# Kernel tuning notes

Measured on AMD Instinct MI355X. Metric: run time of the kernel, lower is better.

The kernel has to match this reference:

```python
import jax, jax.numpy as jnp
import numpy as np

L, R = -0.1, 1.1          # HardKuma stretched support
MAX_REL = 11              # max relative distance
CLAMP_LO, CLAMP_HI = 0.01, 100.0


def setup_inputs() -> dict:
    key = jax.random.key(0)
    ks = jax.random.split(key, 12)
    B, T, Din, Dout = 4, 2048, 512, 256
    s_in = 0.02
    return {
        "q": jax.random.normal(ks[0], (B, T, Din), jnp.float32),
        "k": jax.random.normal(ks[1], (B, T, Din), jnp.float32),
        "Wa1": jax.random.normal(ks[2], (Din, Dout), jnp.float32) * s_in,
        "ba1": jnp.zeros((Dout,), jnp.float32),
        "Wa2": jax.random.normal(ks[3], (Dout, Dout), jnp.float32) * s_in,
        "ba2": jnp.zeros((Dout,), jnp.float32),
        "Wb1": jax.random.normal(ks[4], (Din, Dout), jnp.float32) * s_in,
        "bb1": jnp.zeros((Dout,), jnp.float32),
        "Wb2": jax.random.normal(ks[5], (Dout, Dout), jnp.float32) * s_in,
        "bb2": jnp.zeros((Dout,), jnp.float32),
        "dist_emb": jax.random.normal(ks[6], (2 * MAX_REL + 1,), jnp.float32) * 0.02,
    }


def _mlp(x, W1, b1, W2, b2):
    # Sequential(Linear, ReLU, Dropout, Linear, ReLU, Dropout) in eval mode
    h = jax.nn.relu(x @ W1 + b1)
    return jax.nn.relu(h @ W2 + b2)


def _rel_dists(T, dist_emb):
    i = jnp.arange(T)
    rel = jnp.clip(i[None, :] - i[:, None], -MAX_REL, MAX_REL) + MAX_REL  # [T,T] ints in [0,22]
    return dist_emb[rel]  # [T,T]


def _kuma_cdf(t, a, b):
    # F(t; a, b) = 1 - (1 - t^a)^b, t is a positive Python-float constant
    return 1.0 - jnp.power(1.0 - jnp.power(t, a), b)


def _kuma_mean(a, b):
    # E[X] = b * Beta(1 + 1/a, b)
    g = 1.0 + 1.0 / a
    return b * jnp.exp(jax.scipy.special.gammaln(g) + jax.scipy.special.gammaln(b)
                       - jax.scipy.special.gammaln(g + b))


def reference(q, k, Wa1, ba1, Wa2, ba2, Wb1, bb1, Wb2, bb2, dist_emb):
    T = q.shape[1]
    q_a = _mlp(q, Wa1, ba1, Wa2, ba2)
    k_a = _mlp(k, Wa1, ba1, Wa2, ba2)
    q_b = _mlp(q, Wb1, bb1, Wb2, bb2)
    k_b = _mlp(k, Wb1, bb1, Wb2, bb2)

    a = jnp.einsum("btd,bsd->bts", q_a, k_a)  # [B,T,T]
    b = jnp.einsum("btd,bsd->bts", q_b, k_b)

    rd = _rel_dists(T, dist_emb)[None]  # [1,T,T]
    a = a + rd
    b = b + rd

    a = jnp.clip(jax.nn.softplus(a), CLAMP_LO, CLAMP_HI)
    b = jnp.clip(jax.nn.softplus(b), CLAMP_LO, CLAMP_HI)

    # HardKuma deterministic (eval) attention
    t0 = (0.0 - L) / (R - L)  # stretched coord of 0
    t1 = (1.0 - L) / (R - L)  # stretched coord of 1
    p0 = _kuma_cdf(t0, a, b)          # P(h = 0)
    p1 = 1.0 - _kuma_cdf(t1, a, b)    # P(h = 1)
    pc = 1.0 - p0 - p1                # continuous mass

    mean = jnp.clip(L + (R - L) * _kuma_mean(a, b), 0.0, 1.0)
    zero_one = jnp.where(p0 > p1, 0.0, 1.0)
    att = jnp.where(pc < 0.5, zero_one, mean)
    return att
```

## Files before the change

### kernel.cpp

```cpp
#include <hip/hip_runtime.h>
#include <hip/hip_bf16.h>
#include <math.h>

typedef __hip_bfloat16 bf16;
typedef short bf16x8 __attribute__((ext_vector_type(8)));
typedef float f32x4 __attribute__((ext_vector_type(4)));
typedef float f32x2 __attribute__((ext_vector_type(2)));

union alignas(16) Pack8 { bf16 h[8]; bf16x8 v; };

#define EXP2F(x) __builtin_amdgcn_exp2f(x)
#define LOG2F(x) __builtin_amdgcn_logf(x)
#define RCPF(x)  __builtin_amdgcn_rcpf(x)

#define TAB_N   64
#define TAB_LO  (-0.35f)
#define TAB_HI  (1.25f)
#define TAB_STRIDE 65

__global__ void prep_weights(const float* __restrict__ Wa1, const float* __restrict__ Wa2,
                             const float* __restrict__ Wb1, const float* __restrict__ Wb2,
                             bf16* __restrict__ oa1, bf16* __restrict__ oa2,
                             bf16* __restrict__ ob1, bf16* __restrict__ ob2) {
    int idx = blockIdx.x * 256 + threadIdx.x;
    if (idx < 131072) {
        int n = idx >> 9, k = idx & 511;
        oa1[idx] = __float2bfloat16(Wa1[k * 256 + n]);
    } else if (idx < 196608) {
        int i = idx - 131072; int n = i >> 8, k = i & 255;
        oa2[i] = __float2bfloat16(Wa2[k * 256 + n]);
    } else if (idx < 327680) {
        int i = idx - 196608; int n = i >> 9, k = i & 511;
        ob1[i] = __float2bfloat16(Wb1[k * 256 + n]);
    } else {
        int i = idx - 327680; int n = i >> 8, k = i & 255;
        ob2[i] = __float2bfloat16(Wb2[k * 256 + n]);
    }
}

__device__ __forceinline__ float stirl2s(float z) {
    float iz = 1.f / z;
    return (z - 0.5f) * LOG2F(z) - 1.44269504f * z + 1.32574806f
         + iz * (0.12022651f - 0.00400749f * iz * iz);
}
__device__ __forceinline__ float sp4s(float x) {
    return (x * (x + 1.f)) * ((x + 2.f) * (x + 3.f));
}
__device__ float mean_f32(float sa, float sb) {
    float lw = LOG2F(1.f + EXP2F(sa * 1.44269504f));
    float lv = LOG2F(1.f + EXP2F(sb * 1.44269504f));
    lw = fminf(fmaxf(lw, 0.01442695f), 144.269504f);
    lv = fminf(fmaxf(lv, 0.01442695f), 144.269504f);
    float b = 0.69314718f * lv;
    float g = 1.44269504f / lw + 1.f;
    float gb = g + b;
    float lb2 = stirl2s(g + 4.f) + stirl2s(b + 4.f) - stirl2s(gb + 4.f)
              + LOG2F(sp4s(gb) / (sp4s(g) * sp4s(b)));
    float mean = fmaf(1.2f * b, EXP2F(lb2), -0.1f);
    return fminf(fmaxf(mean, 0.f), 1.f);
}

__global__ void gen_table(float* __restrict__ tab) {
    int idx = blockIdx.x * 256 + threadIdx.x;
    if (idx >= TAB_N * TAB_N) return;
    int ia = idx >> 6, ib = idx & 63;
    const float step = (TAB_HI - TAB_LO) / (TAB_N - 1);
    float sa  = TAB_LO + ia * step;
    float sb  = TAB_LO + ib * step;
    int ib1 = ib < TAB_N - 1 ? ib + 1 : ib;
    float sb1 = TAB_LO + ib1 * step;
    tab[(ia * TAB_STRIDE + ib) * 2]     = mean_f32(sa, sb);
    tab[(ia * TAB_STRIDE + ib) * 2 + 1] = mean_f32(sa, sb1);
}

__global__ __launch_bounds__(256, 2)
void mlp_fused(const float* __restrict__ q, const float* __restrict__ k,
               const bf16* __restrict__ Wa1t, const bf16* __restrict__ Wa2t,
               const bf16* __restrict__ Wb1t, const bf16* __restrict__ Wb2t,
               bf16* __restrict__ qa, bf16* __restrict__ ka,
               bf16* __restrict__ qb, bf16* __restrict__ kb) {
    const int z = blockIdx.z;
    const float* X  = (z & 1) ? k : q;
    const bf16*  W1 = (z >> 1) ? Wb1t : Wa1t;
    const bf16*  W2 = (z >> 1) ? Wb2t : Wa2t;
    bf16* Y = (z == 0) ? qa : (z == 1) ? ka : (z == 2) ? qb : kb;
    const int m0 = blockIdx.x * 64;

    __shared__ short lA[64 * 40];
    __shared__ short lB[256 * 40];
    __shared__ short lH[64 * 264];

    const int tid  = threadIdx.x;
    const int wave = tid >> 6, lane = tid & 63;
    const int wn = wave * 64;
    const int quad = lane >> 4, r16 = lane & 15;

    {
        f32x4 acc[4][4] = {};
        for (int kk = 0; kk < 512; kk += 32) {
            {
                int r = tid >> 2, c = (tid & 3) * 8;
                const float* p = X + (size_t)(m0 + r) * 512 + kk + c;
                Pack8 u;
#pragma unroll
                for (int j = 0; j < 8; j++) u.h[j] = __float2bfloat16(p[j]);
                *(bf16x8*)&lA[r * 40 + c] = u.v;
            }
            for (int i = tid; i < 1024; i += 256) {
                int r = i >> 2, c = (i & 3) * 8;
                *(bf16x8*)&lB[r * 40 + c] =
                    *(const bf16x8*)(W1 + (size_t)r * 512 + kk + c);
            }
            __syncthreads();
            bf16x8 af[4], bfr[4];
#pragma unroll
            for (int f = 0; f < 4; f++) {
                af[f]  = *(const bf16x8*)&lA[(f * 16 + r16) * 40 + quad * 8];
                bfr[f] = *(const bf16x8*)&lB[(wn + f * 16 + r16) * 40 + quad * 8];
            }
#pragma unroll
            for (int i = 0; i < 4; i++)
#pragma unroll
                for (int j = 0; j < 4; j++)
                    acc[i][j] = __builtin_amdgcn_mfma_f32_16x16x32_bf16(
                        af[i], bfr[j], acc[i][j], 0, 0, 0);
            __syncthreads();
        }
#pragma unroll
        for (int i = 0; i < 4; i++)
#pragma unroll
            for (int j = 0; j < 4; j++)
#pragma unroll
                for (int r = 0; r < 4; r++) {
                    float v = acc[i][j][r];
                    v = v > 0.f ? v : 0.f;
                    ((bf16*)lH)[(i * 16 + quad * 4 + r) * 264 + wn + j * 16 + r16] =
                        __float2bfloat16(v);
                }
    }
    __syncthreads();

    f32x4 acc2[4][4] = {};
    for (int kk = 0; kk < 256; kk += 32) {
        for (int i = tid; i < 1024; i += 256) {
            int r = i >> 2, c = (i & 3) * 8;
            *(bf16x8*)&lB[r * 40 + c] =
                *(const bf16x8*)(W2 + (size_t)r * 256 + kk + c);
        }
        __syncthreads();
        bf16x8 af[4], bfr[4];
#pragma unroll
        for (int f = 0; f < 4; f++) {
            af[f]  = *(const bf16x8*)&lH[(f * 16 + r16) * 264 + kk + quad * 8];
            bfr[f] = *(const bf16x8*)&lB[(wn + f * 16 + r16) * 40 + quad * 8];
        }
#pragma unroll
        for (int i = 0; i < 4; i++)
#pragma unroll
            for (int j = 0; j < 4; j++)
                acc2[i][j] = __builtin_amdgcn_mfma_f32_16x16x32_bf16(
                    af[i], bfr[j], acc2[i][j], 0, 0, 0);
        __syncthreads();
    }

#pragma unroll
    for (int i = 0; i < 4; i++) {
        int rbase = m0 + i * 16 + quad * 4;
#pragma unroll
        for (int j = 0; j < 4; j++) {
            int col = wn + j * 16 + r16;
#pragma unroll
            for (int r = 0; r < 4; r++) {
                float v = acc2[i][j][r];
                v = v > 0.f ? v : 0.f;
                Y[(size_t)(rbase + r) * 256 + col] = __float2bfloat16(v);
            }
        }
    }
}

__device__ __forceinline__ f32x2 vexp2(f32x2 x) {
    f32x2 r; r.x = EXP2F(x.x); r.y = EXP2F(x.y); return r;
}
__device__ __forceinline__ f32x2 vlog2(f32x2 x) {
    f32x2 r; r.x = LOG2F(x.x); r.y = LOG2F(x.y); return r;
}
__device__ __forceinline__ f32x2 vrcp(f32x2 x) {
    f32x2 r; r.x = RCPF(x.x); r.y = RCPF(x.y); return r;
}
__device__ __forceinline__ f32x2 vclamp(f32x2 x, float lo, float hi) {
    f32x2 r;
    r.x = fminf(fmaxf(x.x, lo), hi);
    r.y = fminf(fmaxf(x.y, lo), hi);
    return r;
}

__device__ __noinline__ f32x2 hardkuma_slow(f32x2 la, f32x2 lb) {
    const float LOG2E = 1.44269504f;
    f32x2 lw = vlog2(1.f + vexp2(la * LOG2E));
    f32x2 lv = vlog2(1.f + vexp2(lb * LOG2E));
    lw = vclamp(lw, 0.01442695f, 144.269504f);
    lv = vclamp(lv, 0.01442695f, 144.269504f);
    f32x2 b = 0.69314718f * lv;

    f32x2 t0a = vexp2(-2.48490665f * lw);
    f32x2 t1a = vexp2(-0.08701138f * lw);
    f32x2 q0 = vexp2(b * vlog2(1.f - t0a));
    f32x2 p1 = vexp2(b * vlog2(1.f - t1a));
    f32x2 pc = q0 - p1;
    f32x2 p0 = 1.f - q0;

    f32x2 g  = 1.44269504f * vrcp(lw) + 1.f;
    f32x2 gb = g + b;
    f32x2 g2 = g + 2.f, b2 = b + 2.f, gb2 = gb + 2.f;

    f32x2 s = (g + 1.5f) * vlog2(g2) + (b + 1.5f) * vlog2(b2)
            - (gb + 1.5f) * vlog2(gb2);

    const float C1 = 0.12022459f;
    const float C2 = -0.00400749f;
    f32x2 pg  = g2 * b2;
    f32x2 rr3 = vrcp(pg * gb2);
    f32x2 ig  = rr3 * (b2 * gb2);
    f32x2 ib  = rr3 * (g2 * gb2);
    f32x2 igb = rr3 * pg;
    f32x2 corr = ig  * (C1 + C2 * (ig  * ig))
               + ib  * (C1 + C2 * (ib  * ib))
               - igb * (C1 + C2 * (igb * igb));
    s += corr - 1.55964202f;

    f32x2 ng = g * (g + 1.f), nb = b * (b + 1.f), ngb = gb * (gb + 1.f);
    s += vlog2(ngb * vrcp(ng * nb));

    f32x2 mean = (1.2f * b) * vexp2(s) - 0.1f;
    mean = vclamp(mean, 0.f, 1.f);

    f32x2 att;
    att.x = (pc.x < 0.5f) ? ((p0.x > p1.x) ? 0.f : 1.f) : mean.x;
    att.y = (pc.y < 0.5f) ? ((p0.y > p1.y) ? 0.f : 1.f) : mean.y;
    return att;
}

__global__ __launch_bounds__(256, 2)
void kuma_attn(const bf16* __restrict__ qa, const bf16* __restrict__ ka,
               const bf16* __restrict__ qb, const bf16* __restrict__ kb,
               const float* __restrict__ dist_emb, const float* __restrict__ tabg,
               float* __restrict__ out) {
    const int bidx = blockIdx.z;
    const int t0 = blockIdx.x * 128;
    const int s0 = blockIdx.y * 128;

    __shared__ short lQa[128 * 40], lQb[128 * 40];
    __shared__ short lKa[128 * 40], lKb[128 * 40];
    __shared__ float sDist[23];
    __shared__ float sTab[TAB_N * TAB_STRIDE * 2];

    const int tid = threadIdx.x;
    if (tid < 23) sDist[tid] = dist_emb[tid];
    for (int i = tid; i < (TAB_N * TAB_STRIDE * 2) / 4; i += 256)
        ((f32x4*)sTab)[i] = ((const f32x4*)tabg)[i];

    const int wave = tid >> 6, lane = tid & 63;
    const int wm = (wave >> 1) * 64, wn = (wave & 1) * 64;
    const int quad = lane >> 4, r16 = lane & 15;
    const size_t base = (size_t)bidx * 2048 * 256;

    f32x4 accA[4][4] = {};
    f32x4 accB[4][4] = {};

    const int r0 = tid >> 2, c0 = (tid & 3) * 8;
    const int r1 = r0 + 64,  c1 = c0;

    for (int kk = 0; kk < 256; kk += 32) {
        {
            size_t gq0 = base + (size_t)(t0 + r0) * 256 + kk + c0;
            size_t gq1 = base + (size_t)(t0 + r1) * 256 + kk + c1;
            *(bf16x8*)&lQa[r0 * 40 + c0] = *(const bf16x8*)(qa + gq0);
            *(bf16x8*)&lQb[r0 * 40 + c0] = *(const bf16x8*)(qb + gq0);
            *(bf16x8*)&lQa[r1 * 40 + c1] = *(const bf16x8*)(qa + gq1);
            *(bf16x8*)&lQb[r1 * 40 + c1] = *(const bf16x8*)(qb + gq1);
            size_t gk0 = base + (size_t)(s0 + r0) * 256 + kk + c0;
            size_t gk1 = base + (size_t)(s0 + r1) * 256 + kk + c1;
            *(bf16x8*)&lKa[r0 * 40 + c0] = *(const bf16x8*)(ka + gk0);
            *(bf16x8*)&lKb[r0 * 40 + c0] = *(const bf16x8*)(kb + gk0);
            *(bf16x8*)&lKa[r1 * 40 + c1] = *(const bf16x8*)(ka + gk1);
            *(bf16x8*)&lKb[r1 * 40 + c1] = *(const bf16x8*)(kb + gk1);
        }
        __syncthreads();
        bf16x8 aA[4], aB[4], bA[4], bB[4];
#pragma unroll
        for (int f = 0; f < 4; f++) {
            int ar = (wm + f * 16 + r16) * 40 + quad * 8;
            aA[f] = *(const bf16x8*)&lQa[ar];
            aB[f] = *(const bf16x8*)&lQb[ar];
            int br = (wn + f * 16 + r16) * 40 + quad * 8;
            bA[f] = *(const bf16x8*)&lKa[br];
            bB[f] = *(const bf16x8*)&lKb[br];
        }
#pragma unroll
        for (int i = 0; i < 4; i++)
#pragma unroll
            for (int j = 0; j < 4; j++) {
                accA[i][j] = __builtin_amdgcn_mfma_f32_16x16x32_bf16(
                    aA[i], bA[j], accA[i][j], 0, 0, 0);
                accB[i][j] = __builtin_amdgcn_mfma_f32_16x16x32_bf16(
                    aB[i], bB[j], accB[i][j], 0, 0, 0);
            }
        __syncthreads();
    }

    const float SCALE = (TAB_N - 1) / (TAB_HI - TAB_LO);
#pragma unroll
    for (int i = 0; i < 4; i++) {
#pragma unroll
        for (int j = 0; j < 4; j++) {
            int s = s0 + wn + j * 16 + r16;
#pragma unroll
            for (int rr = 0; rr < 2; rr++) {
                int t = t0 + wm + i * 16 + quad * 4 + rr * 2;
                int d0 = s - t;
                int d1 = d0 - 1;
                d0 = d0 < -11 ? -11 : (d0 > 11 ? 11 : d0);
                d1 = d1 < -11 ? -11 : (d1 > 11 ? 11 : d1);
                float rd0 = sDist[d0 + 11];
                float rd1 = sDist[d1 + 11];
                f32x2 la  = { accA[i][j][rr * 2] + rd0, accA[i][j][rr * 2 + 1] + rd1 };
                f32x2 lbv = { accB[i][j][rr * 2] + rd0, accB[i][j][rr * 2 + 1] + rd1 };

                float mn = fminf(fminf(la.x, la.y), fminf(lbv.x, lbv.y));
                float mx = fmaxf(fmaxf(la.x, la.y), fmaxf(lbv.x, lbv.y));

                f32x2 u = vclamp((la  - TAB_LO) * SCALE, 0.f, (float)(TAB_N - 1));
                f32x2 v = vclamp((lbv - TAB_LO) * SCALE, 0.f, (float)(TAB_N - 1));
                int ia0 = (int)u.x; ia0 = ia0 > TAB_N - 2 ? TAB_N - 2 : ia0;
                int ia1 = (int)u.y; ia1 = ia1 > TAB_N - 2 ? TAB_N - 2 : ia1;
                int ib0 = (int)v.x; ib0 = ib0 > TAB_N - 2 ? TAB_N - 2 : ib0;
                int ib1 = (int)v.y; ib1 = ib1 > TAB_N - 2 ? TAB_N - 2 : ib1;
                f32x2 fa = { u.x - (float)ia0, u.y - (float)ia1 };
                f32x2 fb = { v.x - (float)ib0, v.y - (float)ib1 };
                int o0 = (ia0 * TAB_STRIDE + ib0) * 2;
                int o1 = (ia1 * TAB_STRIDE + ib1) * 2;
                f32x2 e0r0 = *(const f32x2*)&sTab[o0];
                f32x2 e0r1 = *(const f32x2*)&sTab[o0 + TAB_STRIDE * 2];
                f32x2 e1r0 = *(const f32x2*)&sTab[o1];
                f32x2 e1r1 = *(const f32x2*)&sTab[o1 + TAB_STRIDE * 2];
                f32x2 m0 = { e0r0.x + fb.x * (e0r0.y - e0r0.x),
                             e1r0.x + fb.y * (e1r0.y - e1r0.x) };
                f32x2 m1 = { e0r1.x + fb.x * (e0r1.y - e0r1.x),
                             e1r1.x + fb.y * (e1r1.y - e1r1.x) };
                f32x2 att = m0 + fa * (m1 - m0);

                bool oob = (mn < TAB_LO) | (mx > TAB_HI);
                if (__builtin_expect(__any(oob), 0)) {
                    f32x2 ex = hardkuma_slow(la, lbv);
                    if (oob) att = ex;
                }

                out[((size_t)bidx * 2048 + t) * 2048 + s] = att.x;
                out[((size_t)bidx * 2048 + t + 1) * 2048 + s] = att.y;
            }
        }
    }
}

extern "C" void kernel_launch(void* const* d_in, const int* in_sizes, int n_in,
                              void* d_out, int out_size, void* d_ws, size_t ws_size,
                              hipStream_t stream) {
    const float* q    = (const float*)d_in[0];
    const float* k    = (const float*)d_in[1];
    const float* Wa1  = (const float*)d_in[2];
    const float* Wa2  = (const float*)d_in[4];
    const float* Wb1  = (const float*)d_in[6];
    const float* Wb2  = (const float*)d_in[8];
    const float* dist = (const float*)d_in[10];
    float* out = (float*)d_out;

    bf16* wsbf = (bf16*)d_ws;
    bf16* Wa1t = wsbf;
    bf16* Wa2t = Wa1t + 131072;
    bf16* Wb1t = Wa2t + 65536;
    bf16* Wb2t = Wb1t + 131072;
    bf16* qa   = Wb2t + 65536;
    bf16* ka   = qa + 2097152;
    bf16* qb   = ka + 2097152;
    bf16* kb   = qb + 2097152;
    float* tabg = (float*)Wa1t;

    prep_weights<<<1536, 256, 0, stream>>>(Wa1, Wa2, Wb1, Wb2,
                                           Wa1t, Wa2t, Wb1t, Wb2t);

    dim3 g1(128, 1, 4), blk(256, 1, 1);
    mlp_fused<<<g1, blk, 0, stream>>>(q, k, Wa1t, Wa2t, Wb1t, Wb2t,
                                      qa, ka, qb, kb);

    gen_table<<<16, 256, 0, stream>>>(tabg);

    dim3 g2(16, 16, 4);
    kuma_attn<<<g2, blk, 0, stream>>>(qa, ka, qb, kb, dist, tabg, out);
}
```

Measured before the change: 197.0 us.

## Merge table generation into weight prep, load MLP operands directly, prefetch attention tiles

```diff
diff --git a/kernel.cpp b/kernel.cpp
--- a/kernel.cpp
+++ b/kernel.cpp
@@ -18,10 +18,46 @@
 #define TAB_HI  (1.25f)
 #define TAB_STRIDE 65
 
+__device__ __forceinline__ float stirl2s(float z) {
+    float iz = 1.f / z;
+    return (z - 0.5f) * LOG2F(z) - 1.44269504f * z + 1.32574806f
+         + iz * (0.12022651f - 0.00400749f * iz * iz);
+}
+__device__ __forceinline__ float sp4s(float x) {
+    return (x * (x + 1.f)) * ((x + 2.f) * (x + 3.f));
+}
+__device__ float mean_f32(float sa, float sb) {
+    float lw = LOG2F(1.f + EXP2F(sa * 1.44269504f));
+    float lv = LOG2F(1.f + EXP2F(sb * 1.44269504f));
+    lw = fminf(fmaxf(lw, 0.01442695f), 144.269504f);
+    lv = fminf(fmaxf(lv, 0.01442695f), 144.269504f);
+    float b = 0.69314718f * lv;
+    float g = 1.44269504f / lw + 1.f;
+    float gb = g + b;
+    float lb2 = stirl2s(g + 4.f) + stirl2s(b + 4.f) - stirl2s(gb + 4.f)
+              + LOG2F(sp4s(gb) / (sp4s(g) * sp4s(b)));
+    float mean = fmaf(1.2f * b, EXP2F(lb2), -0.1f);
+    return fminf(fmaxf(mean, 0.f), 1.f);
+}
+
 __global__ void prep_weights(const float* __restrict__ Wa1, const float* __restrict__ Wa2,
                              const float* __restrict__ Wb1, const float* __restrict__ Wb2,
                              bf16* __restrict__ oa1, bf16* __restrict__ oa2,
-                             bf16* __restrict__ ob1, bf16* __restrict__ ob2) {
+                             bf16* __restrict__ ob1, bf16* __restrict__ ob2,
+                             float* __restrict__ tab) {
+    if (blockIdx.x >= 1536) {
+        int idx = (blockIdx.x - 1536) * 256 + threadIdx.x;
+        if (idx >= TAB_N * TAB_N) return;
+        int ia = idx >> 6, ib = idx & 63;
+        const float step = (TAB_HI - TAB_LO) / (TAB_N - 1);
+        float sa  = TAB_LO + ia * step;
+        float sb  = TAB_LO + ib * step;
+        int ib1 = ib < TAB_N - 1 ? ib + 1 : ib;
+        float sb1 = TAB_LO + ib1 * step;
+        tab[(ia * TAB_STRIDE + ib) * 2]     = mean_f32(sa, sb);
+        tab[(ia * TAB_STRIDE + ib) * 2 + 1] = mean_f32(sa, sb1);
+        return;
+    }
     int idx = blockIdx.x * 256 + threadIdx.x;
     if (idx < 131072) {
         int n = idx >> 9, k = idx & 511;
@@ -38,42 +74,7 @@
     }
 }
 
-__device__ __forceinline__ float stirl2s(float z) {
-    float iz = 1.f / z;
-    return (z - 0.5f) * LOG2F(z) - 1.44269504f * z + 1.32574806f
-         + iz * (0.12022651f - 0.00400749f * iz * iz);
-}
-__device__ __forceinline__ float sp4s(float x) {
-    return (x * (x + 1.f)) * ((x + 2.f) * (x + 3.f));
-}
-__device__ float mean_f32(float sa, float sb) {
-    float lw = LOG2F(1.f + EXP2F(sa * 1.44269504f));
-    float lv = LOG2F(1.f + EXP2F(sb * 1.44269504f));
-    lw = fminf(fmaxf(lw, 0.01442695f), 144.269504f);
-    lv = fminf(fmaxf(lv, 0.01442695f), 144.269504f);
-    float b = 0.69314718f * lv;
-    float g = 1.44269504f / lw + 1.f;
-    float gb = g + b;
-    float lb2 = stirl2s(g + 4.f) + stirl2s(b + 4.f) - stirl2s(gb + 4.f)
-              + LOG2F(sp4s(gb) / (sp4s(g) * sp4s(b)));
-    float mean = fmaf(1.2f * b, EXP2F(lb2), -0.1f);
-    return fminf(fmaxf(mean, 0.f), 1.f);
-}
-
-__global__ void gen_table(float* __restrict__ tab) {
-    int idx = blockIdx.x * 256 + threadIdx.x;
-    if (idx >= TAB_N * TAB_N) return;
-    int ia = idx >> 6, ib = idx & 63;
-    const float step = (TAB_HI - TAB_LO) / (TAB_N - 1);
-    float sa  = TAB_LO + ia * step;
-    float sb  = TAB_LO + ib * step;
-    int ib1 = ib < TAB_N - 1 ? ib + 1 : ib;
-    float sb1 = TAB_LO + ib1 * step;
-    tab[(ia * TAB_STRIDE + ib) * 2]     = mean_f32(sa, sb);
-    tab[(ia * TAB_STRIDE + ib) * 2 + 1] = mean_f32(sa, sb1);
-}
-
-__global__ __launch_bounds__(256, 2)
+__global__ __launch_bounds__(256, 3)
 void mlp_fused(const float* __restrict__ q, const float* __restrict__ k,
                const bf16* __restrict__ Wa1t, const bf16* __restrict__ Wa2t,
                const bf16* __restrict__ Wb1t, const bf16* __restrict__ Wb2t,
@@ -86,8 +87,6 @@
     bf16* Y = (z == 0) ? qa : (z == 1) ? ka : (z == 2) ? qb : kb;
     const int m0 = blockIdx.x * 64;
 
-    __shared__ short lA[64 * 40];
-    __shared__ short lB[256 * 40];
     __shared__ short lH[64 * 264];
 
     const int tid  = threadIdx.x;
@@ -97,26 +96,19 @@
 
     {
         f32x4 acc[4][4] = {};
+        const float* xb = X + (size_t)(m0 + r16) * 512 + quad * 8;
+        const bf16*  wb = W1 + (size_t)(wn + r16) * 512 + quad * 8;
+#pragma unroll 4
         for (int kk = 0; kk < 512; kk += 32) {
-            {
-                int r = tid >> 2, c = (tid & 3) * 8;
-                const float* p = X + (size_t)(m0 + r) * 512 + kk + c;
+            bf16x8 af[4], bfr[4];
+#pragma unroll
+            for (int f = 0; f < 4; f++) {
+                const float* p = xb + (size_t)f * 16 * 512 + kk;
                 Pack8 u;
 #pragma unroll
                 for (int j = 0; j < 8; j++) u.h[j] = __float2bfloat16(p[j]);
-                *(bf16x8*)&lA[r * 40 + c] = u.v;
-            }
-            for (int i = tid; i < 1024; i += 256) {
-                int r = i >> 2, c = (i & 3) * 8;
-                *(bf16x8*)&lB[r * 40 + c] =
-                    *(const bf16x8*)(W1 + (size_t)r * 512 + kk + c);
-            }
-            __syncthreads();
-            bf16x8 af[4], bfr[4];
-#pragma unroll
-            for (int f = 0; f < 4; f++) {
-                af[f]  = *(const bf16x8*)&lA[(f * 16 + r16) * 40 + quad * 8];
-                bfr[f] = *(const bf16x8*)&lB[(wn + f * 16 + r16) * 40 + quad * 8];
+                af[f] = u.v;
+                bfr[f] = *(const bf16x8*)(wb + (size_t)f * 16 * 512 + kk);
             }
 #pragma unroll
             for (int i = 0; i < 4; i++)
@@ -124,7 +116,6 @@
                 for (int j = 0; j < 4; j++)
                     acc[i][j] = __builtin_amdgcn_mfma_f32_16x16x32_bf16(
                         af[i], bfr[j], acc[i][j], 0, 0, 0);
-            __syncthreads();
         }
 #pragma unroll
         for (int i = 0; i < 4; i++)
@@ -141,26 +132,23 @@
     __syncthreads();
 
     f32x4 acc2[4][4] = {};
-    for (int kk = 0; kk < 256; kk += 32) {
-        for (int i = tid; i < 1024; i += 256) {
-            int r = i >> 2, c = (i & 3) * 8;
-            *(bf16x8*)&lB[r * 40 + c] =
-                *(const bf16x8*)(W2 + (size_t)r * 256 + kk + c);
+    {
+        const bf16* wb = W2 + (size_t)(wn + r16) * 256 + quad * 8;
+#pragma unroll 2
+        for (int kk = 0; kk < 256; kk += 32) {
+            bf16x8 af[4], bfr[4];
+#pragma unroll
+            for (int f = 0; f < 4; f++) {
+                af[f]  = *(const bf16x8*)&lH[(f * 16 + r16) * 264 + kk + quad * 8];
+                bfr[f] = *(const bf16x8*)(wb + (size_t)f * 16 * 256 + kk);
+            }
+#pragma unroll
+            for (int i = 0; i < 4; i++)
+#pragma unroll
+                for (int j = 0; j < 4; j++)
+                    acc2[i][j] = __builtin_amdgcn_mfma_f32_16x16x32_bf16(
+                        af[i], bfr[j], acc2[i][j], 0, 0, 0);
         }
-        __syncthreads();
-        bf16x8 af[4], bfr[4];
-#pragma unroll
-        for (int f = 0; f < 4; f++) {
-            af[f]  = *(const bf16x8*)&lH[(f * 16 + r16) * 264 + kk + quad * 8];
-            bfr[f] = *(const bf16x8*)&lB[(wn + f * 16 + r16) * 40 + quad * 8];
-        }
-#pragma unroll
-        for (int i = 0; i < 4; i++)
-#pragma unroll
-            for (int j = 0; j < 4; j++)
-                acc2[i][j] = __builtin_amdgcn_mfma_f32_16x16x32_bf16(
-                    af[i], bfr[j], acc2[i][j], 0, 0, 0);
-        __syncthreads();
     }
 
 #pragma unroll
@@ -269,24 +257,37 @@
     f32x4 accB[4][4] = {};
 
     const int r0 = tid >> 2, c0 = (tid & 3) * 8;
-    const int r1 = r0 + 64,  c1 = c0;
-
+    const int r1 = r0 + 64;
+
+    bf16x8 rQa0, rQa1, rQb0, rQb1, rKa0, rKa1, rKb0, rKb1;
+    auto prefetch = [&](int kk) {
+        size_t gq0 = base + (size_t)(t0 + r0) * 256 + kk + c0;
+        size_t gq1 = base + (size_t)(t0 + r1) * 256 + kk + c0;
+        size_t gk0 = base + (size_t)(s0 + r0) * 256 + kk + c0;
+        size_t gk1 = base + (size_t)(s0 + r1) * 256 + kk + c0;
+        rQa0 = *(const bf16x8*)(qa + gq0);
+        rQa1 = *(const bf16x8*)(qa + gq1);
+        rQb0 = *(const bf16x8*)(qb + gq0);
+        rQb1 = *(const bf16x8*)(qb + gq1);
+        rKa0 = *(const bf16x8*)(ka + gk0);
+        rKa1 = *(const bf16x8*)(ka + gk1);
+        rKb0 = *(const bf16x8*)(kb + gk0);
+        rKb1 = *(const bf16x8*)(kb + gk1);
+    };
+    prefetch(0);
+
+#pragma unroll
     for (int kk = 0; kk < 256; kk += 32) {
-        {
-            size_t gq0 = base + (size_t)(t0 + r0) * 256 + kk + c0;
-            size_t gq1 = base + (size_t)(t0 + r1) * 256 + kk + c1;
-            *(bf16x8*)&lQa[r0 * 40 + c0] = *(const bf16x8*)(qa + gq0);
-            *(bf16x8*)&lQb[r0 * 40 + c0] = *(const bf16x8*)(qb + gq0);
-            *(bf16x8*)&lQa[r1 * 40 + c1] = *(const bf16x8*)(qa + gq1);
-            *(bf16x8*)&lQb[r1 * 40 + c1] = *(const bf16x8*)(qb + gq1);
-            size_t gk0 = base + (size_t)(s0 + r0) * 256 + kk + c0;
-            size_t gk1 = base + (size_t)(s0 + r1) * 256 + kk + c1;
-            *(bf16x8*)&lKa[r0 * 40 + c0] = *(const bf16x8*)(ka + gk0);
-            *(bf16x8*)&lKb[r0 * 40 + c0] = *(const bf16x8*)(kb + gk0);
-            *(bf16x8*)&lKa[r1 * 40 + c1] = *(const bf16x8*)(ka + gk1);
-            *(bf16x8*)&lKb[r1 * 40 + c1] = *(const bf16x8*)(kb + gk1);
-        }
+        *(bf16x8*)&lQa[r0 * 40 + c0] = rQa0;
+        *(bf16x8*)&lQa[r1 * 40 + c0] = rQa1;
+        *(bf16x8*)&lQb[r0 * 40 + c0] = rQb0;
+        *(bf16x8*)&lQb[r1 * 40 + c0] = rQb1;
+        *(bf16x8*)&lKa[r0 * 40 + c0] = rKa0;
+        *(bf16x8*)&lKa[r1 * 40 + c0] = rKa1;
+        *(bf16x8*)&lKb[r0 * 40 + c0] = rKb0;
+        *(bf16x8*)&lKb[r1 * 40 + c0] = rKb1;
         __syncthreads();
+        if (kk < 224) prefetch(kk + 32);
         bf16x8 aA[4], aB[4], bA[4], bB[4];
 #pragma unroll
         for (int f = 0; f < 4; f++) {
@@ -384,17 +385,16 @@
     bf16* ka   = qa + 2097152;
     bf16* qb   = ka + 2097152;
     bf16* kb   = qb + 2097152;
-    float* tabg = (float*)Wa1t;
-
-    prep_weights<<<1536, 256, 0, stream>>>(Wa1, Wa2, Wb1, Wb2,
-                                           Wa1t, Wa2t, Wb1t, Wb2t);
+    bf16* tabr = kb + 2097152;
+    float* tabg = (float*)tabr;
+
+    prep_weights<<<1552, 256, 0, stream>>>(Wa1, Wa2, Wb1, Wb2,
+                                           Wa1t, Wa2t, Wb1t, Wb2t, tabg);
 
     dim3 g1(128, 1, 4), blk(256, 1, 1);
     mlp_fused<<<g1, blk, 0, stream>>>(q, k, Wa1t, Wa2t, Wb1t, Wb2t,
                                       qa, ka, qb, kb);
 
-    gen_table<<<16, 256, 0, stream>>>(tabg);
-
     dim3 g2(16, 16, 4);
     kuma_attn<<<g2, blk, 0, stream>>>(qa, ka, qb, kb, dist, tabg, out);
 }
```

Result: slower. 211.9 us (+7.6%).

## Fuse all stages into one persistent kernel with atomic grid barriers

Applied to the files above, without the earlier changes.

```diff
diff --git a/kernel.cpp b/kernel.cpp
--- a/kernel.cpp
+++ b/kernel.cpp
@@ -18,25 +18,8 @@
 #define TAB_HI  (1.25f)
 #define TAB_STRIDE 65
 
-__global__ void prep_weights(const float* __restrict__ Wa1, const float* __restrict__ Wa2,
-                             const float* __restrict__ Wb1, const float* __restrict__ Wb2,
-                             bf16* __restrict__ oa1, bf16* __restrict__ oa2,
-                             bf16* __restrict__ ob1, bf16* __restrict__ ob2) {
-    int idx = blockIdx.x * 256 + threadIdx.x;
-    if (idx < 131072) {
-        int n = idx >> 9, k = idx & 511;
-        oa1[idx] = __float2bfloat16(Wa1[k * 256 + n]);
-    } else if (idx < 196608) {
-        int i = idx - 131072; int n = i >> 8, k = i & 255;
-        oa2[i] = __float2bfloat16(Wa2[k * 256 + n]);
-    } else if (idx < 327680) {
-        int i = idx - 196608; int n = i >> 9, k = i & 511;
-        ob1[i] = __float2bfloat16(Wb1[k * 256 + n]);
-    } else {
-        int i = idx - 327680; int n = i >> 8, k = i & 255;
-        ob2[i] = __float2bfloat16(Wb2[k * 256 + n]);
-    }
-}
+#define NBLK 512
+
 
 __device__ __forceinline__ float stirl2s(float z) {
     float iz = 1.f / z;
@@ -60,125 +43,6 @@
     return fminf(fmaxf(mean, 0.f), 1.f);
 }
 
-__global__ void gen_table(float* __restrict__ tab) {
-    int idx = blockIdx.x * 256 + threadIdx.x;
-    if (idx >= TAB_N * TAB_N) return;
-    int ia = idx >> 6, ib = idx & 63;
-    const float step = (TAB_HI - TAB_LO) / (TAB_N - 1);
-    float sa  = TAB_LO + ia * step;
-    float sb  = TAB_LO + ib * step;
-    int ib1 = ib < TAB_N - 1 ? ib + 1 : ib;
-    float sb1 = TAB_LO + ib1 * step;
-    tab[(ia * TAB_STRIDE + ib) * 2]     = mean_f32(sa, sb);
-    tab[(ia * TAB_STRIDE + ib) * 2 + 1] = mean_f32(sa, sb1);
-}
-
-__global__ __launch_bounds__(256, 2)
-void mlp_fused(const float* __restrict__ q, const float* __restrict__ k,
-               const bf16* __restrict__ Wa1t, const bf16* __restrict__ Wa2t,
-               const bf16* __restrict__ Wb1t, const bf16* __restrict__ Wb2t,
-               bf16* __restrict__ qa, bf16* __restrict__ ka,
-               bf16* __restrict__ qb, bf16* __restrict__ kb) {
-    const int z = blockIdx.z;
-    const float* X  = (z & 1) ? k : q;
-    const bf16*  W1 = (z >> 1) ? Wb1t : Wa1t;
-    const bf16*  W2 = (z >> 1) ? Wb2t : Wa2t;
-    bf16* Y = (z == 0) ? qa : (z == 1) ? ka : (z == 2) ? qb : kb;
-    const int m0 = blockIdx.x * 64;
-
-    __shared__ short lA[64 * 40];
-    __shared__ short lB[256 * 40];
-    __shared__ short lH[64 * 264];
-
-    const int tid  = threadIdx.x;
-    const int wave = tid >> 6, lane = tid & 63;
-    const int wn = wave * 64;
-    const int quad = lane >> 4, r16 = lane & 15;
-
-    {
-        f32x4 acc[4][4] = {};
-        for (int kk = 0; kk < 512; kk += 32) {
-            {
-                int r = tid >> 2, c = (tid & 3) * 8;
-                const float* p = X + (size_t)(m0 + r) * 512 + kk + c;
-                Pack8 u;
-#pragma unroll
-                for (int j = 0; j < 8; j++) u.h[j] = __float2bfloat16(p[j]);
-                *(bf16x8*)&lA[r * 40 + c] = u.v;
-            }
-            for (int i = tid; i < 1024; i += 256) {
-                int r = i >> 2, c = (i & 3) * 8;
-                *(bf16x8*)&lB[r * 40 + c] =
-                    *(const bf16x8*)(W1 + (size_t)r * 512 + kk + c);
-            }
-            __syncthreads();
-            bf16x8 af[4], bfr[4];
-#pragma unroll
-            for (int f = 0; f < 4; f++) {
-                af[f]  = *(const bf16x8*)&lA[(f * 16 + r16) * 40 + quad * 8];
-                bfr[f] = *(const bf16x8*)&lB[(wn + f * 16 + r16) * 40 + quad * 8];
-            }
-#pragma unroll
-            for (int i = 0; i < 4; i++)
-#pragma unroll
-                for (int j = 0; j < 4; j++)
-                    acc[i][j] = __builtin_amdgcn_mfma_f32_16x16x32_bf16(
-                        af[i], bfr[j], acc[i][j], 0, 0, 0);
-            __syncthreads();
-        }
-#pragma unroll
-        for (int i = 0; i < 4; i++)
-#pragma unroll
-            for (int j = 0; j < 4; j++)
-#pragma unroll
-                for (int r = 0; r < 4; r++) {
-                    float v = acc[i][j][r];
-                    v = v > 0.f ? v : 0.f;
-                    ((bf16*)lH)[(i * 16 + quad * 4 + r) * 264 + wn + j * 16 + r16] =
-                        __float2bfloat16(v);
-                }
-    }
-    __syncthreads();
-
-    f32x4 acc2[4][4] = {};
-    for (int kk = 0; kk < 256; kk += 32) {
-        for (int i = tid; i < 1024; i += 256) {
-            int r = i >> 2, c = (i & 3) * 8;
-            *(bf16x8*)&lB[r * 40 + c] =
-                *(const bf16x8*)(W2 + (size_t)r * 256 + kk + c);
-        }
-        __syncthreads();
-        bf16x8 af[4], bfr[4];
-#pragma unroll
-        for (int f = 0; f < 4; f++) {
-            af[f]  = *(const bf16x8*)&lH[(f * 16 + r16) * 264 + kk + quad * 8];
-            bfr[f] = *(const bf16x8*)&lB[(wn + f * 16 + r16) * 40 + quad * 8];
-        }
-#pragma unroll
-        for (int i = 0; i < 4; i++)
-#pragma unroll
-            for (int j = 0; j < 4; j++)
-                acc2[i][j] = __builtin_amdgcn_mfma_f32_16x16x32_bf16(
-                    af[i], bfr[j], acc2[i][j], 0, 0, 0);
-        __syncthreads();
-    }
-
-#pragma unroll
-    for (int i = 0; i < 4; i++) {
-        int rbase = m0 + i * 16 + quad * 4;
-#pragma unroll
-        for (int j = 0; j < 4; j++) {
-            int col = wn + j * 16 + r16;
-#pragma unroll
-            for (int r = 0; r < 4; r++) {
-                float v = acc2[i][j][r];
-                v = v > 0.f ? v : 0.f;
-                Y[(size_t)(rbase + r) * 256 + col] = __float2bfloat16(v);
-            }
-        }
-    }
-}
-
 __device__ __forceinline__ f32x2 vexp2(f32x2 x) {
     f32x2 r; r.x = EXP2F(x.x); r.y = EXP2F(x.y); return r;
 }
@@ -241,123 +105,297 @@
     return att;
 }
 
+__device__ __forceinline__ void grid_sync(unsigned* cnt) {
+    __syncthreads();
+    if (threadIdx.x == 0) {
+        __threadfence();
+        atomicAdd(cnt, 1u);
+        while (atomicAdd(cnt, 0u) < NBLK) __builtin_amdgcn_s_sleep(8);
+        __threadfence();
+    }
+    __syncthreads();
+}
+
+__device__ __forceinline__ void transpose_tile(const float* __restrict__ src,
+                                               bf16* __restrict__ dst,
+                                               int K, int N, int kt, int nt,
+                                               float* tile ) {
+    const int tid = threadIdx.x;
+    const int tx = tid & 31, ty = tid >> 5;
+    const int k0 = kt * 32, n0 = nt * 32;
+#pragma unroll
+    for (int i = 0; i < 4; i++)
+        tile[(ty + 8 * i) * 33 + tx] = src[(size_t)(k0 + ty + 8 * i) * N + n0 + tx];
+    __syncthreads();
+#pragma unroll
+    for (int i = 0; i < 4; i++)
+        dst[(size_t)(n0 + ty + 8 * i) * K + k0 + tx] =
+            __float2bfloat16(tile[tx * 33 + ty + 8 * i]);
+}
+
 __global__ __launch_bounds__(256, 2)
-void kuma_attn(const bf16* __restrict__ qa, const bf16* __restrict__ ka,
-               const bf16* __restrict__ qb, const bf16* __restrict__ kb,
-               const float* __restrict__ dist_emb, const float* __restrict__ tabg,
+void fused_all(const float* __restrict__ q, const float* __restrict__ k,
+               const float* __restrict__ Wa1, const float* __restrict__ Wa2,
+               const float* __restrict__ Wb1, const float* __restrict__ Wb2,
+               const float* __restrict__ dist_emb,
+               bf16* __restrict__ Wa1t, bf16* __restrict__ Wa2t,
+               bf16* __restrict__ Wb1t, bf16* __restrict__ Wb2t,
+               bf16* __restrict__ qa, bf16* __restrict__ ka,
+               bf16* __restrict__ qb, bf16* __restrict__ kb,
+               float* __restrict__ tabg, unsigned* __restrict__ cnts,
                float* __restrict__ out) {
-    const int bidx = blockIdx.z;
-    const int t0 = blockIdx.x * 128;
-    const int s0 = blockIdx.y * 128;
-
-    __shared__ short lQa[128 * 40], lQb[128 * 40];
-    __shared__ short lKa[128 * 40], lKb[128 * 40];
-    __shared__ float sDist[23];
-    __shared__ float sTab[TAB_N * TAB_STRIDE * 2];
-
-    const int tid = threadIdx.x;
-    if (tid < 23) sDist[tid] = dist_emb[tid];
-    for (int i = tid; i < (TAB_N * TAB_STRIDE * 2) / 4; i += 256)
-        ((f32x4*)sTab)[i] = ((const f32x4*)tabg)[i];
-
-    const int wave = tid >> 6, lane = tid & 63;
-    const int wm = (wave >> 1) * 64, wn = (wave & 1) * 64;
-    const int quad = lane >> 4, r16 = lane & 15;
-    const size_t base = (size_t)bidx * 2048 * 256;
-
-    f32x4 accA[4][4] = {};
-    f32x4 accB[4][4] = {};
-
-    const int r0 = tid >> 2, c0 = (tid & 3) * 8;
-    const int r1 = r0 + 64,  c1 = c0;
-
-    for (int kk = 0; kk < 256; kk += 32) {
+    __shared__ alignas(16) char smem[74336];
+    const int tid  = threadIdx.x;
+    const int wgid = blockIdx.x;
+
+    {
+        float* tile = (float*)smem;
+        if (wgid < 128) {
+            transpose_tile(Wa1, Wa1t, 512, 256, wgid >> 3, wgid & 7, tile);
+        } else if (wgid < 192) {
+            int u = wgid - 128;
+            transpose_tile(Wa2, Wa2t, 256, 256, u >> 3, u & 7, tile);
+        } else if (wgid < 320) {
+            int u = wgid - 192;
+            transpose_tile(Wb1, Wb1t, 512, 256, u >> 3, u & 7, tile);
+        } else if (wgid < 384) {
+            int u = wgid - 320;
+            transpose_tile(Wb2, Wb2t, 256, 256, u >> 3, u & 7, tile);
+        } else if (wgid < 400) {
+            int idx = (wgid - 384) * 256 + tid;
+            int ia = idx >> 6, ib = idx & 63;
+            const float step = (TAB_HI - TAB_LO) / (TAB_N - 1);
+            float sa  = TAB_LO + ia * step;
+            float sb  = TAB_LO + ib * step;
+            int ib1 = ib < TAB_N - 1 ? ib + 1 : ib;
+            float sb1 = TAB_LO + ib1 * step;
+            tabg[(ia * TAB_STRIDE + ib) * 2]     = mean_f32(sa, sb);
+            tabg[(ia * TAB_STRIDE + ib) * 2 + 1] = mean_f32(sa, sb1);
+        }
+    }
+    grid_sync(cnts);
+
+    {
+        short* lA = (short*)smem;
+        short* lB = (short*)(smem + 5120);
+        short* lH = (short*)(smem + 25600);
+
+        const int z = wgid >> 7;
+        const float* X  = (z & 1) ? k : q;
+        const bf16*  W1 = (z >> 1) ? Wb1t : Wa1t;
+        const bf16*  W2 = (z >> 1) ? Wb2t : Wa2t;
+        bf16* Y = (z == 0) ? qa : (z == 1) ? ka : (z == 2) ? qb : kb;
+        const int m0 = (wgid & 127) * 64;
+
+        const int wave = tid >> 6, lane = tid & 63;
+        const int wn = wave * 64;
+        const int quad = lane >> 4, r16 = lane & 15;
+
         {
-            size_t gq0 = base + (size_t)(t0 + r0) * 256 + kk + c0;
-            size_t gq1 = base + (size_t)(t0 + r1) * 256 + kk + c1;
-            *(bf16x8*)&lQa[r0 * 40 + c0] = *(const bf16x8*)(qa + gq0);
-            *(bf16x8*)&lQb[r0 * 40 + c0] = *(const bf16x8*)(qb + gq0);
-            *(bf16x8*)&lQa[r1 * 40 + c1] = *(const bf16x8*)(qa + gq1);
-            *(bf16x8*)&lQb[r1 * 40 + c1] = *(const bf16x8*)(qb + gq1);
-            size_t gk0 = base + (size_t)(s0 + r0) * 256 + kk + c0;
-            size_t gk1 = base + (size_t)(s0 + r1) * 256 + kk + c1;
-            *(bf16x8*)&lKa[r0 * 40 + c0] = *(const bf16x8*)(ka + gk0);
-            *(bf16x8*)&lKb[r0 * 40 + c0] = *(const bf16x8*)(kb + gk0);
-            *(bf16x8*)&lKa[r1 * 40 + c1] = *(const bf16x8*)(ka + gk1);
-            *(bf16x8*)&lKb[r1 * 40 + c1] = *(const bf16x8*)(kb + gk1);
+            f32x4 acc[4][4] = {};
+            for (int kk = 0; kk < 512; kk += 32) {
+                {
+                    int r = tid >> 2, c = (tid & 3) * 8;
+                    const float* p = X + (size_t)(m0 + r) * 512 + kk + c;
+                    Pack8 u;
+#pragma unroll
+                    for (int j = 0; j < 8; j++) u.h[j] = __float2bfloat16(p[j]);
+                    *(bf16x8*)&lA[r * 40 + c] = u.v;
+                }
+                for (int i = tid; i < 1024; i += 256) {
+                    int r = i >> 2, c = (i & 3) * 8;
+                    *(bf16x8*)&lB[r * 40 + c] =
+                        *(const bf16x8*)(W1 + (size_t)r * 512 + kk + c);
+                }
+                __syncthreads();
+                bf16x8 af[4], bfr[4];
+#pragma unroll
+                for (int f = 0; f < 4; f++) {
+                    af[f]  = *(const bf16x8*)&lA[(f * 16 + r16) * 40 + quad * 8];
+                    bfr[f] = *(const bf16x8*)&lB[(wn + f * 16 + r16) * 40 + quad * 8];
+                }
+#pragma unroll
+                for (int i = 0; i < 4; i++)
+#pragma unroll
+                    for (int j = 0; j < 4; j++)
+                        acc[i][j] = __builtin_amdgcn_mfma_f32_16x16x32_bf16(
+                            af[i], bfr[j], acc[i][j], 0, 0, 0);
+                __syncthreads();
+            }
+#pragma unroll
+            for (int i = 0; i < 4; i++)
+#pragma unroll
+                for (int j = 0; j < 4; j++)
+#pragma unroll
+                    for (int r = 0; r < 4; r++) {
+                        float v = acc[i][j][r];
+                        v = v > 0.f ? v : 0.f;
+                        ((bf16*)lH)[(i * 16 + quad * 4 + r) * 264 + wn + j * 16 + r16] =
+                            __float2bfloat16(v);
+                    }
         }
         __syncthreads();
-        bf16x8 aA[4], aB[4], bA[4], bB[4];
-#pragma unroll
-        for (int f = 0; f < 4; f++) {
-            int ar = (wm + f * 16 + r16) * 40 + quad * 8;
-            aA[f] = *(const bf16x8*)&lQa[ar];
-            aB[f] = *(const bf16x8*)&lQb[ar];
-            int br = (wn + f * 16 + r16) * 40 + quad * 8;
-            bA[f] = *(const bf16x8*)&lKa[br];
-            bB[f] = *(const bf16x8*)&lKb[br];
+
+        f32x4 acc2[4][4] = {};
+        for (int kk = 0; kk < 256; kk += 32) {
+            for (int i = tid; i < 1024; i += 256) {
+                int r = i >> 2, c = (i & 3) * 8;
+                *(bf16x8*)&lB[r * 40 + c] =
+                    *(const bf16x8*)(W2 + (size_t)r * 256 + kk + c);
+            }
+            __syncthreads();
+            bf16x8 af[4], bfr[4];
+#pragma unroll
+            for (int f = 0; f < 4; f++) {
+                af[f]  = *(const bf16x8*)&lH[(f * 16 + r16) * 264 + kk + quad * 8];
+                bfr[f] = *(const bf16x8*)&lB[(wn + f * 16 + r16) * 40 + quad * 8];
+            }
+#pragma unroll
+            for (int i = 0; i < 4; i++)
+#pragma unroll
+                for (int j = 0; j < 4; j++)
+                    acc2[i][j] = __builtin_amdgcn_mfma_f32_16x16x32_bf16(
+                        af[i], bfr[j], acc2[i][j], 0, 0, 0);
+            __syncthreads();
         }
-#pragma unroll
-        for (int i = 0; i < 4; i++)
+
+#pragma unroll
+        for (int i = 0; i < 4; i++) {
+            int rbase = m0 + i * 16 + quad * 4;
 #pragma unroll
             for (int j = 0; j < 4; j++) {
-                accA[i][j] = __builtin_amdgcn_mfma_f32_16x16x32_bf16(
-                    aA[i], bA[j], accA[i][j], 0, 0, 0);
-                accB[i][j] = __builtin_amdgcn_mfma_f32_16x16x32_bf16(
-                    aB[i], bB[j], accB[i][j], 0, 0, 0);
-            }
-        __syncthreads();
+                int col = wn + j * 16 + r16;
+#pragma unroll
+                for (int r = 0; r < 4; r++) {
+                    float v = acc2[i][j][r];
+                    v = v > 0.f ? v : 0.f;
+                    Y[(size_t)(rbase + r) * 256 + col] = __float2bfloat16(v);
+                }
+            }
+        }
     }
-
-    const float SCALE = (TAB_N - 1) / (TAB_HI - TAB_LO);
-#pragma unroll
-    for (int i = 0; i < 4; i++) {
-#pragma unroll
-        for (int j = 0; j < 4; j++) {
-            int s = s0 + wn + j * 16 + r16;
-#pragma unroll
-            for (int rr = 0; rr < 2; rr++) {
-                int t = t0 + wm + i * 16 + quad * 4 + rr * 2;
-                int d0 = s - t;
-                int d1 = d0 - 1;
-                d0 = d0 < -11 ? -11 : (d0 > 11 ? 11 : d0);
-                d1 = d1 < -11 ? -11 : (d1 > 11 ? 11 : d1);
-                float rd0 = sDist[d0 + 11];
-                float rd1 = sDist[d1 + 11];
-                f32x2 la  = { accA[i][j][rr * 2] + rd0, accA[i][j][rr * 2 + 1] + rd1 };
-                f32x2 lbv = { accB[i][j][rr * 2] + rd0, accB[i][j][rr * 2 + 1] + rd1 };
-
-                float mn = fminf(fminf(la.x, la.y), fminf(lbv.x, lbv.y));
-                float mx = fmaxf(fmaxf(la.x, la.y), fmaxf(lbv.x, lbv.y));
-
-                f32x2 u = vclamp((la  - TAB_LO) * SCALE, 0.f, (float)(TAB_N - 1));
-                f32x2 v = vclamp((lbv - TAB_LO) * SCALE, 0.f, (float)(TAB_N - 1));
-                int ia0 = (int)u.x; ia0 = ia0 > TAB_N - 2 ? TAB_N - 2 : ia0;
-                int ia1 = (int)u.y; ia1 = ia1 > TAB_N - 2 ? TAB_N - 2 : ia1;
-                int ib0 = (int)v.x; ib0 = ib0 > TAB_N - 2 ? TAB_N - 2 : ib0;
-                int ib1 = (int)v.y; ib1 = ib1 > TAB_N - 2 ? TAB_N - 2 : ib1;
-                f32x2 fa = { u.x - (float)ia0, u.y - (float)ia1 };
-                f32x2 fb = { v.x - (float)ib0, v.y - (float)ib1 };
-                int o0 = (ia0 * TAB_STRIDE + ib0) * 2;
-                int o1 = (ia1 * TAB_STRIDE + ib1) * 2;
-                f32x2 e0r0 = *(const f32x2*)&sTab[o0];
-                f32x2 e0r1 = *(const f32x2*)&sTab[o0 + TAB_STRIDE * 2];
-                f32x2 e1r0 = *(const f32x2*)&sTab[o1];
-                f32x2 e1r1 = *(const f32x2*)&sTab[o1 + TAB_STRIDE * 2];
-                f32x2 m0 = { e0r0.x + fb.x * (e0r0.y - e0r0.x),
-                             e1r0.x + fb.y * (e1r0.y - e1r0.x) };
-                f32x2 m1 = { e0r1.x + fb.x * (e0r1.y - e0r1.x),
-                             e1r1.x + fb.y * (e1r1.y - e1r1.x) };
-                f32x2 att = m0 + fa * (m1 - m0);
-
-                bool oob = (mn < TAB_LO) | (mx > TAB_HI);
-                if (__builtin_expect(__any(oob), 0)) {
-                    f32x2 ex = hardkuma_slow(la, lbv);
-                    if (oob) att = ex;
-                }
-
-                out[((size_t)bidx * 2048 + t) * 2048 + s] = att.x;
-                out[((size_t)bidx * 2048 + t + 1) * 2048 + s] = att.y;
+    grid_sync(cnts + 1);
+
+    {
+        short* lQa = (short*)smem;
+        short* lQb = (short*)(smem + 10240);
+        short* lKa = (short*)(smem + 20480);
+        short* lKb = (short*)(smem + 30720);
+        float* sTab  = (float*)(smem + 40960);
+        float* sDist = (float*)(smem + 74240);
+
+        if (tid < 23) sDist[tid] = dist_emb[tid];
+        for (int i = tid; i < (TAB_N * TAB_STRIDE * 2) / 4; i += 256)
+            ((f32x4*)sTab)[i] = ((const f32x4*)tabg)[i];
+
+        const int wave = tid >> 6, lane = tid & 63;
+        const int wm = (wave >> 1) * 64, wn = (wave & 1) * 64;
+        const int quad = lane >> 4, r16 = lane & 15;
+        const int r0 = tid >> 2, c0 = (tid & 3) * 8;
+        const int r1 = r0 + 64;
+        const float SCALE = (TAB_N - 1) / (TAB_HI - TAB_LO);
+
+        for (int tt = 0; tt < 2; tt++) {
+            const int tile = wgid * 2 + tt;
+            const int bidx = tile >> 8;
+            const int rem  = tile & 255;
+            const int t0 = (rem >> 4) * 128;
+            const int s0 = (rem & 15) * 128;
+            const size_t base = (size_t)bidx * 2048 * 256;
+
+            f32x4 accA[4][4] = {};
+            f32x4 accB[4][4] = {};
+
+            for (int kk = 0; kk < 256; kk += 32) {
+                {
+                    size_t gq0 = base + (size_t)(t0 + r0) * 256 + kk + c0;
+                    size_t gq1 = base + (size_t)(t0 + r1) * 256 + kk + c0;
+                    *(bf16x8*)&lQa[r0 * 40 + c0] = *(const bf16x8*)(qa + gq0);
+                    *(bf16x8*)&lQb[r0 * 40 + c0] = *(const bf16x8*)(qb + gq0);
+                    *(bf16x8*)&lQa[r1 * 40 + c0] = *(const bf16x8*)(qa + gq1);
+                    *(bf16x8*)&lQb[r1 * 40 + c0] = *(const bf16x8*)(qb + gq1);
+                    size_t gk0 = base + (size_t)(s0 + r0) * 256 + kk + c0;
+                    size_t gk1 = base + (size_t)(s0 + r1) * 256 + kk + c0;
+                    *(bf16x8*)&lKa[r0 * 40 + c0] = *(const bf16x8*)(ka + gk0);
+                    *(bf16x8*)&lKb[r0 * 40 + c0] = *(const bf16x8*)(kb + gk0);
+                    *(bf16x8*)&lKa[r1 * 40 + c0] = *(const bf16x8*)(ka + gk1);
+                    *(bf16x8*)&lKb[r1 * 40 + c0] = *(const bf16x8*)(kb + gk1);
+                }
+                __syncthreads();
+                bf16x8 aA[4], aB[4], bA[4], bB[4];
+#pragma unroll
+                for (int f = 0; f < 4; f++) {
+                    int ar = (wm + f * 16 + r16) * 40 + quad * 8;
+                    aA[f] = *(const bf16x8*)&lQa[ar];
+                    aB[f] = *(const bf16x8*)&lQb[ar];
+                    int br = (wn + f * 16 + r16) * 40 + quad * 8;
+                    bA[f] = *(const bf16x8*)&lKa[br];
+                    bB[f] = *(const bf16x8*)&lKb[br];
+                }
+#pragma unroll
+                for (int i = 0; i < 4; i++)
+#pragma unroll
+                    for (int j = 0; j < 4; j++) {
+                        accA[i][j] = __builtin_amdgcn_mfma_f32_16x16x32_bf16(
+                            aA[i], bA[j], accA[i][j], 0, 0, 0);
+                        accB[i][j] = __builtin_amdgcn_mfma_f32_16x16x32_bf16(
+                            aB[i], bB[j], accB[i][j], 0, 0, 0);
+                    }
+                __syncthreads();
+            }
+
+#pragma unroll
+            for (int i = 0; i < 4; i++) {
+#pragma unroll
+                for (int j = 0; j < 4; j++) {
+                    int s = s0 + wn + j * 16 + r16;
+#pragma unroll
+                    for (int rr = 0; rr < 2; rr++) {
+                        int t = t0 + wm + i * 16 + quad * 4 + rr * 2;
+                        int d0 = s - t;
+                        int d1 = d0 - 1;
+                        d0 = d0 < -11 ? -11 : (d0 > 11 ? 11 : d0);
+                        d1 = d1 < -11 ? -11 : (d1 > 11 ? 11 : d1);
+                        float rd0 = sDist[d0 + 11];
+                        float rd1 = sDist[d1 + 11];
+                        f32x2 la  = { accA[i][j][rr * 2] + rd0,
+                                      accA[i][j][rr * 2 + 1] + rd1 };
+                        f32x2 lbv = { accB[i][j][rr * 2] + rd0,
+                                      accB[i][j][rr * 2 + 1] + rd1 };
+
+                        float mn = fminf(fminf(la.x, la.y), fminf(lbv.x, lbv.y));
+                        float mx = fmaxf(fmaxf(la.x, la.y), fmaxf(lbv.x, lbv.y));
+
+                        f32x2 u = vclamp((la  - TAB_LO) * SCALE, 0.f, (float)(TAB_N - 1));
+                        f32x2 v = vclamp((lbv - TAB_LO) * SCALE, 0.f, (float)(TAB_N - 1));
+                        int ia0 = (int)u.x; ia0 = ia0 > TAB_N - 2 ? TAB_N - 2 : ia0;
+                        int ia1 = (int)u.y; ia1 = ia1 > TAB_N - 2 ? TAB_N - 2 : ia1;
+                        int ib0 = (int)v.x; ib0 = ib0 > TAB_N - 2 ? TAB_N - 2 : ib0;
+                        int ib1 = (int)v.y; ib1 = ib1 > TAB_N - 2 ? TAB_N - 2 : ib1;
+                        f32x2 fa = { u.x - (float)ia0, u.y - (float)ia1 };
+                        f32x2 fb = { v.x - (float)ib0, v.y - (float)ib1 };
+                        int o0 = (ia0 * TAB_STRIDE + ib0) * 2;
+                        int o1 = (ia1 * TAB_STRIDE + ib1) * 2;
+                        f32x2 e0r0 = *(const f32x2*)&sTab[o0];
+                        f32x2 e0r1 = *(const f32x2*)&sTab[o0 + TAB_STRIDE * 2];
+                        f32x2 e1r0 = *(const f32x2*)&sTab[o1];
+                        f32x2 e1r1 = *(const f32x2*)&sTab[o1 + TAB_STRIDE * 2];
+                        f32x2 m0 = { e0r0.x + fb.x * (e0r0.y - e0r0.x),
+                                     e1r0.x + fb.y * (e1r0.y - e1r0.x) };
+                        f32x2 m1 = { e0r1.x + fb.x * (e0r1.y - e0r1.x),
+                                     e1r1.x + fb.y * (e1r1.y - e1r1.x) };
+                        f32x2 att = m0 + fa * (m1 - m0);
+
+                        bool oob = (mn < TAB_LO) | (mx > TAB_HI);
+                        if (__builtin_expect(__any(oob), 0)) {
+                            f32x2 ex = hardkuma_slow(la, lbv);
+                            if (oob) att = ex;
+                        }
+
+                        out[((size_t)bidx * 2048 + t) * 2048 + s] = att.x;
+                        out[((size_t)bidx * 2048 + t + 1) * 2048 + s] = att.y;
+                    }
+                }
             }
         }
     }
@@ -384,17 +422,13 @@
     bf16* ka   = qa + 2097152;
     bf16* qb   = ka + 2097152;
     bf16* kb   = qb + 2097152;
-    float* tabg = (float*)Wa1t;
-
-    prep_weights<<<1536, 256, 0, stream>>>(Wa1, Wa2, Wb1, Wb2,
-                                           Wa1t, Wa2t, Wb1t, Wb2t);
-
-    dim3 g1(128, 1, 4), blk(256, 1, 1);
-    mlp_fused<<<g1, blk, 0, stream>>>(q, k, Wa1t, Wa2t, Wb1t, Wb2t,
-                                      qa, ka, qb, kb);
-
-    gen_table<<<16, 256, 0, stream>>>(tabg);
-
-    dim3 g2(16, 16, 4);
-    kuma_attn<<<g2, blk, 0, stream>>>(qa, ka, qb, kb, dist, tabg, out);
-}
+    bf16* tail = kb + 2097152;
+    float* tabg = (float*)tail;
+    unsigned* cnts = (unsigned*)(tabg + TAB_N * TAB_STRIDE * 2);
+
+    hipMemsetAsync(cnts, 0, 2 * sizeof(unsigned), stream);
+
+    fused_all<<<NBLK, 256, 0, stream>>>(q, k, Wa1, Wa2, Wb1, Wb2, dist,
+                                        Wa1t, Wa2t, Wb1t, Wb2t,
+                                        qa, ka, qb, kb, tabg, cnts, out);
+}
```

After: 296.9 us. 1.51x slower.
